# Performance work log

Hardware: AMD Instinct MI355X
Metric: run time of the kernel (lower is better)

## Reference

```python
import jax, jax.numpy as jnp
import numpy as np

# Dimensions per init_kwargs / input_specs
B, N, C = 8192, 4, 2048          # tokens, expansion_rate, hidden_dim
SINKHORN_ITERS = 20
EPS = 1e-5
ALPHA_INIT = 0.01


def setup_inputs() -> dict:
    key = jax.random.key(0)
    k1, k2 = jax.random.split(key)
    return {
        "x_expanded": jax.random.normal(k1, (B, N, C), dtype=jnp.float32),
        "rmsnorm_weight": jnp.ones((C,), dtype=jnp.float32),   # init: ones
        "H_pre": jnp.zeros((N,), dtype=jnp.float32),            # init: zeros
        "H_post": jnp.zeros((N,), dtype=jnp.float32),           # init: zeros
        "H_res": ALPHA_INIT * jax.random.normal(k2, (N, N), dtype=jnp.float32),
    }


def _sinkhorn(M, iters, eps):
    """Iterative row/column normalization -> (approximately) doubly-stochastic."""
    def body(_, M):
        M = M / (jnp.sum(M, axis=1, keepdims=True) + eps)  # row normalize
        M = M / (jnp.sum(M, axis=0, keepdims=True) + eps)  # col normalize
        return M
    return jax.lax.fori_loop(0, iters, body, M)


def reference(x_expanded, rmsnorm_weight, H_pre, H_post, H_res):
    # RMSNorm over hidden dim C, per (token, branch)
    ms = jnp.mean(x_expanded * x_expanded, axis=-1, keepdims=True)  # [B, N, 1]
    x_norm = x_expanded * jax.lax.rsqrt(ms + EPS) * rmsnorm_weight  # [B, N, C]

    # Manifold-constrained residual mixing matrix (doubly stochastic via Sinkhorn)
    H = _sinkhorn(jnp.exp(H_res), SINKHORN_ITERS, EPS)              # [N, N]

    pre = jax.nn.sigmoid(H_pre)    # [N] input-aggregation weights
    post = jax.nn.sigmoid(H_post)  # [N] output-distribution weights

    # Aggregate normalized branches into a single stream, redistribute,
    # and add the Sinkhorn-mixed residual of the raw branches.
    x_agg = jnp.einsum('n,bnc->bc', pre, x_norm)                     # [B, C]
    y = jnp.einsum('mn,bnc->bmc', H, x_expanded) \
        + post[None, :, None] * x_agg[:, None, :]                    # [B, N, C]
    return y
```

## Files before the change

### kernel.cpp

```cpp
#include <hip/hip_runtime.h>
#include <math.h>

#define B_TOK 8192
#define NB 4
#define CH 2048
#define TPB 512
#define SINK_ITERS 20
#define EPS 1e-5f

__global__ void mhc_sinkhorn(const float* __restrict__ H_pre,
                             const float* __restrict__ H_post,
                             const float* __restrict__ H_res,
                             float* __restrict__ ws)
{
    if (threadIdx.x == 0) {
        float M[NB][NB];
        #pragma unroll
        for (int i = 0; i < NB; ++i)
            #pragma unroll
            for (int j = 0; j < NB; ++j)
                M[i][j] = expf(H_res[i * NB + j]);

        for (int it = 0; it < SINK_ITERS; ++it) {
            #pragma unroll
            for (int i = 0; i < NB; ++i) {
                float r = 1.0f / (M[i][0] + M[i][1] + M[i][2] + M[i][3] + EPS);
                #pragma unroll
                for (int j = 0; j < NB; ++j) M[i][j] *= r;
            }
            #pragma unroll
            for (int j = 0; j < NB; ++j) {
                float r = 1.0f / (M[0][j] + M[1][j] + M[2][j] + M[3][j] + EPS);
                #pragma unroll
                for (int i = 0; i < NB; ++i) M[i][j] *= r;
            }
        }
        #pragma unroll
        for (int i = 0; i < NB; ++i)
            #pragma unroll
            for (int j = 0; j < NB; ++j)
                ws[i * NB + j] = M[i][j];
        #pragma unroll
        for (int n = 0; n < NB; ++n) {
            ws[16 + n] = 1.0f / (1.0f + expf(-H_pre[n]));
            ws[20 + n] = 1.0f / (1.0f + expf(-H_post[n]));
        }
    }
}

__global__ __launch_bounds__(TPB) void mhc_main(const float* __restrict__ x,
                                                const float* __restrict__ w,
                                                const float* __restrict__ ws,
                                                float* __restrict__ y)
{
    const int b = blockIdx.x;
    const int t = threadIdx.x;
    const int wave = t >> 6;
    const int lane = t & 63;

    float H[NB][NB], pre[NB], post[NB];
    #pragma unroll
    for (int i = 0; i < NB; ++i)
        #pragma unroll
        for (int j = 0; j < NB; ++j)
            H[i][j] = ws[i * NB + j];
    #pragma unroll
    for (int n = 0; n < NB; ++n) {
        pre[n]  = ws[16 + n];
        post[n] = ws[20 + n];
    }

    const float4* xb = (const float4*)(x + (size_t)b * NB * CH);
    float4 x0 = xb[0 * (CH / 4) + t];
    float4 x1 = xb[1 * (CH / 4) + t];
    float4 x2 = xb[2 * (CH / 4) + t];
    float4 x3 = xb[3 * (CH / 4) + t];

    float4 wv = ((const float4*)w)[t];

    float ss[NB];
    ss[0] = x0.x * x0.x + x0.y * x0.y + x0.z * x0.z + x0.w * x0.w;
    ss[1] = x1.x * x1.x + x1.y * x1.y + x1.z * x1.z + x1.w * x1.w;
    ss[2] = x2.x * x2.x + x2.y * x2.y + x2.z * x2.z + x2.w * x2.w;
    ss[3] = x3.x * x3.x + x3.y * x3.y + x3.z * x3.z + x3.w * x3.w;

    #pragma unroll
    for (int m = 1; m < 64; m <<= 1) {
        #pragma unroll
        for (int n = 0; n < NB; ++n)
            ss[n] += __shfl_xor(ss[n], m);
    }
    __shared__ float red[TPB / 64][NB];
    if (lane == 0) {
        #pragma unroll
        for (int n = 0; n < NB; ++n) red[wave][n] = ss[n];
    }
    __syncthreads();

    float s[NB];
    #pragma unroll
    for (int n = 0; n < NB; ++n) {
        float tot = red[0][n] + red[1][n] + red[2][n] + red[3][n] +
                    red[4][n] + red[5][n] + red[6][n] + red[7][n];
        s[n] = pre[n] * rsqrtf(tot * (1.0f / CH) + EPS);
    }

    float4 wu;
    wu.x = wv.x * (s[0] * x0.x + s[1] * x1.x + s[2] * x2.x + s[3] * x3.x);
    wu.y = wv.y * (s[0] * x0.y + s[1] * x1.y + s[2] * x2.y + s[3] * x3.y);
    wu.z = wv.z * (s[0] * x0.z + s[1] * x1.z + s[2] * x2.z + s[3] * x3.z);
    wu.w = wv.w * (s[0] * x0.w + s[1] * x1.w + s[2] * x2.w + s[3] * x3.w);

    float4* yb = (float4*)(y + (size_t)b * NB * CH);
    #pragma unroll
    for (int m = 0; m < NB; ++m) {
        float4 o;
        o.x = H[m][0] * x0.x + H[m][1] * x1.x + H[m][2] * x2.x + H[m][3] * x3.x + post[m] * wu.x;
        o.y = H[m][0] * x0.y + H[m][1] * x1.y + H[m][2] * x2.y + H[m][3] * x3.y + post[m] * wu.y;
        o.z = H[m][0] * x0.z + H[m][1] * x1.z + H[m][2] * x2.z + H[m][3] * x3.z + post[m] * wu.z;
        o.w = H[m][0] * x0.w + H[m][1] * x1.w + H[m][2] * x2.w + H[m][3] * x3.w + post[m] * wu.w;
        yb[m * (CH / 4) + t] = o;
    }
}

extern "C" void kernel_launch(void* const* d_in, const int* in_sizes, int n_in,
                              void* d_out, int out_size, void* d_ws, size_t ws_size,
                              hipStream_t stream) {
    const float* x      = (const float*)d_in[0];
    const float* wgt    = (const float*)d_in[1];
    const float* h_pre  = (const float*)d_in[2];
    const float* h_post = (const float*)d_in[3];
    const float* h_res  = (const float*)d_in[4];
    float* y  = (float*)d_out;
    float* ws = (float*)d_ws;

    mhc_sinkhorn<<<1, 64, 0, stream>>>(h_pre, h_post, h_res, ws);
    mhc_main<<<B_TOK, TPB, 0, stream>>>(x, wgt, ws, y);
}
```

Measured before the change: 110.0 us.

## Process eight tokens per block with double-buffered loads and nontemporal memory ops

Each block now handles eight tokens instead of one, loading the next token's four branch rows into registers while the current token is reduced and written (two-stage software pipeline). Double-buffered shared reduction slots let one barrier per token suffice. Loads and stores use nontemporal builtins to avoid polluting caches on this streaming workload. This cuts block launch overhead and improves latency hiding, but reduces grid size to 1024 blocks and increases register pressure.

```diff
diff --git a/kernel.cpp b/kernel.cpp
--- a/kernel.cpp
+++ b/kernel.cpp
@@ -5,8 +5,12 @@
 #define NB 4
 #define CH 2048
 #define TPB 512
+#define NBLK 1024
+#define TOK_PER_BLK 8
 #define SINK_ITERS 20
 #define EPS 1e-5f
+
+typedef float f32x4 __attribute__((ext_vector_type(4)));
 
 __global__ void mhc_sinkhorn(const float* __restrict__ H_pre,
                              const float* __restrict__ H_post,
@@ -53,74 +57,112 @@
                                                 const float* __restrict__ ws,
                                                 float* __restrict__ y)
 {
-    const int b = blockIdx.x;
     const int t = threadIdx.x;
     const int wave = t >> 6;
     const int lane = t & 63;
 
-    float H[NB][NB], pre[NB], post[NB];
-    #pragma unroll
-    for (int i = 0; i < NB; ++i)
+    const float H00 = ws[0],  H01 = ws[1],  H02 = ws[2],  H03 = ws[3];
+    const float H10 = ws[4],  H11 = ws[5],  H12 = ws[6],  H13 = ws[7];
+    const float H20 = ws[8],  H21 = ws[9],  H22 = ws[10], H23 = ws[11];
+    const float H30 = ws[12], H31 = ws[13], H32 = ws[14], H33 = ws[15];
+    const float pre0 = ws[16], pre1 = ws[17], pre2 = ws[18], pre3 = ws[19];
+    const float ps0  = ws[20], ps1  = ws[21], ps2  = ws[22], ps3  = ws[23];
+
+    __shared__ f32x4 red4[2][TPB / 64];
+
+    const f32x4 wv = ((const f32x4*)w)[t];
+    const int b0 = blockIdx.x * TOK_PER_BLK;
+
+    auto xload = [&](int b, f32x4& d0, f32x4& d1, f32x4& d2, f32x4& d3) {
+        const f32x4* p = (const f32x4*)x + (size_t)b * (NB * CH / 4) + t;
+        d0 = __builtin_nontemporal_load(p);
+        d1 = __builtin_nontemporal_load(p + (CH / 4));
+        d2 = __builtin_nontemporal_load(p + 2 * (CH / 4));
+        d3 = __builtin_nontemporal_load(p + 3 * (CH / 4));
+    };
+
+    auto process = [&](int b, f32x4 x0, f32x4 x1, f32x4 x2, f32x4 x3, int ph) {
+        float s0 = x0.x * x0.x + x0.y * x0.y + x0.z * x0.z + x0.w * x0.w;
+        float s1 = x1.x * x1.x + x1.y * x1.y + x1.z * x1.z + x1.w * x1.w;
+        float s2 = x2.x * x2.x + x2.y * x2.y + x2.z * x2.z + x2.w * x2.w;
+        float s3 = x3.x * x3.x + x3.y * x3.y + x3.z * x3.z + x3.w * x3.w;
         #pragma unroll
-        for (int j = 0; j < NB; ++j)
-            H[i][j] = ws[i * NB + j];
-    #pragma unroll
-    for (int n = 0; n < NB; ++n) {
-        pre[n]  = ws[16 + n];
-        post[n] = ws[20 + n];
-    }
+        for (int m = 1; m < 64; m <<= 1) {
+            s0 += __shfl_xor(s0, m);
+            s1 += __shfl_xor(s1, m);
+            s2 += __shfl_xor(s2, m);
+            s3 += __shfl_xor(s3, m);
+        }
+        if (lane == 0) {
+            f32x4 v = { s0, s1, s2, s3 };
+            red4[ph][wave] = v;
+        }
 
-    const float4* xb = (const float4*)(x + (size_t)b * NB * CH);
-    float4 x0 = xb[0 * (CH / 4) + t];
-    float4 x1 = xb[1 * (CH / 4) + t];
-    float4 x2 = xb[2 * (CH / 4) + t];
-    float4 x3 = xb[3 * (CH / 4) + t];
+        __builtin_amdgcn_sched_barrier(0);
+        asm volatile("s_waitcnt lgkmcnt(0)" ::: "memory");
+        __builtin_amdgcn_s_barrier();
+        __builtin_amdgcn_sched_barrier(0);
 
-    float4 wv = ((const float4*)w)[t];
+        f32x4 r0 = red4[ph][0], r1 = red4[ph][1], r2 = red4[ph][2], r3 = red4[ph][3];
+        f32x4 r4 = red4[ph][4], r5 = red4[ph][5], r6 = red4[ph][6], r7 = red4[ph][7];
+        float t0 = ((r0.x + r1.x) + (r2.x + r3.x)) + ((r4.x + r5.x) + (r6.x + r7.x));
+        float t1 = ((r0.y + r1.y) + (r2.y + r3.y)) + ((r4.y + r5.y) + (r6.y + r7.y));
+        float t2 = ((r0.z + r1.z) + (r2.z + r3.z)) + ((r4.z + r5.z) + (r6.z + r7.z));
+        float t3 = ((r0.w + r1.w) + (r2.w + r3.w)) + ((r4.w + r5.w) + (r6.w + r7.w));
 
-    float ss[NB];
-    ss[0] = x0.x * x0.x + x0.y * x0.y + x0.z * x0.z + x0.w * x0.w;
-    ss[1] = x1.x * x1.x + x1.y * x1.y + x1.z * x1.z + x1.w * x1.w;
-    ss[2] = x2.x * x2.x + x2.y * x2.y + x2.z * x2.z + x2.w * x2.w;
-    ss[3] = x3.x * x3.x + x3.y * x3.y + x3.z * x3.z + x3.w * x3.w;
+        const float a0 = pre0 * rsqrtf(t0 * (1.0f / CH) + EPS);
+        const float a1 = pre1 * rsqrtf(t1 * (1.0f / CH) + EPS);
+        const float a2 = pre2 * rsqrtf(t2 * (1.0f / CH) + EPS);
+        const float a3 = pre3 * rsqrtf(t3 * (1.0f / CH) + EPS);
 
-    #pragma unroll
-    for (int m = 1; m < 64; m <<= 1) {
-        #pragma unroll
-        for (int n = 0; n < NB; ++n)
-            ss[n] += __shfl_xor(ss[n], m);
-    }
-    __shared__ float red[TPB / 64][NB];
-    if (lane == 0) {
-        #pragma unroll
-        for (int n = 0; n < NB; ++n) red[wave][n] = ss[n];
-    }
-    __syncthreads();
+        f32x4 wu;
+        wu.x = wv.x * (a0 * x0.x + a1 * x1.x + a2 * x2.x + a3 * x3.x);
+        wu.y = wv.y * (a0 * x0.y + a1 * x1.y + a2 * x2.y + a3 * x3.y);
+        wu.z = wv.z * (a0 * x0.z + a1 * x1.z + a2 * x2.z + a3 * x3.z);
+        wu.w = wv.w * (a0 * x0.w + a1 * x1.w + a2 * x2.w + a3 * x3.w);
 
-    float s[NB];
-    #pragma unroll
-    for (int n = 0; n < NB; ++n) {
-        float tot = red[0][n] + red[1][n] + red[2][n] + red[3][n] +
-                    red[4][n] + red[5][n] + red[6][n] + red[7][n];
-        s[n] = pre[n] * rsqrtf(tot * (1.0f / CH) + EPS);
-    }
+        f32x4* yp = (f32x4*)y + (size_t)b * (NB * CH / 4) + t;
+        f32x4 o;
+        o.x = H00 * x0.x + H01 * x1.x + H02 * x2.x + H03 * x3.x + ps0 * wu.x;
+        o.y = H00 * x0.y + H01 * x1.y + H02 * x2.y + H03 * x3.y + ps0 * wu.y;
+        o.z = H00 * x0.z + H01 * x1.z + H02 * x2.z + H03 * x3.z + ps0 * wu.z;
+        o.w = H00 * x0.w + H01 * x1.w + H02 * x2.w + H03 * x3.w + ps0 * wu.w;
+        __builtin_nontemporal_store(o, yp);
+        o.x = H10 * x0.x + H11 * x1.x + H12 * x2.x + H13 * x3.x + ps1 * wu.x;
+        o.y = H10 * x0.y + H11 * x1.y + H12 * x2.y + H13 * x3.y + ps1 * wu.y;
+        o.z = H10 * x0.z + H11 * x1.z + H12 * x2.z + H13 * x3.z + ps1 * wu.z;
+        o.w = H10 * x0.w + H11 * x1.w + H12 * x2.w + H13 * x3.w + ps1 * wu.w;
+        __builtin_nontemporal_store(o, yp + (CH / 4));
+        o.x = H20 * x0.x + H21 * x1.x + H22 * x2.x + H23 * x3.x + ps2 * wu.x;
+        o.y = H20 * x0.y + H21 * x1.y + H22 * x2.y + H23 * x3.y + ps2 * wu.y;
+        o.z = H20 * x0.z + H21 * x1.z + H22 * x2.z + H23 * x3.z + ps2 * wu.z;
+        o.w = H20 * x0.w + H21 * x1.w + H22 * x2.w + H23 * x3.w + ps2 * wu.w;
+        __builtin_nontemporal_store(o, yp + 2 * (CH / 4));
+        o.x = H30 * x0.x + H31 * x1.x + H32 * x2.x + H33 * x3.x + ps3 * wu.x;
+        o.y = H30 * x0.y + H31 * x1.y + H32 * x2.y + H33 * x3.y + ps3 * wu.y;
+        o.z = H30 * x0.z + H31 * x1.z + H32 * x2.z + H33 * x3.z + ps3 * wu.z;
+        o.w = H30 * x0.w + H31 * x1.w + H32 * x2.w + H33 * x3.w + ps3 * wu.w;
+        __builtin_nontemporal_store(o, yp + 3 * (CH / 4));
+    };
 
-    float4 wu;
-    wu.x = wv.x * (s[0] * x0.x + s[1] * x1.x + s[2] * x2.x + s[3] * x3.x);
-    wu.y = wv.y * (s[0] * x0.y + s[1] * x1.y + s[2] * x2.y + s[3] * x3.y);
-    wu.z = wv.z * (s[0] * x0.z + s[1] * x1.z + s[2] * x2.z + s[3] * x3.z);
-    wu.w = wv.w * (s[0] * x0.w + s[1] * x1.w + s[2] * x2.w + s[3] * x3.w);
+    f32x4 xA0, xA1, xA2, xA3, xB0, xB1, xB2, xB3;
 
-    float4* yb = (float4*)(y + (size_t)b * NB * CH);
-    #pragma unroll
-    for (int m = 0; m < NB; ++m) {
-        float4 o;
-        o.x = H[m][0] * x0.x + H[m][1] * x1.x + H[m][2] * x2.x + H[m][3] * x3.x + post[m] * wu.x;
-        o.y = H[m][0] * x0.y + H[m][1] * x1.y + H[m][2] * x2.y + H[m][3] * x3.y + post[m] * wu.y;
-        o.z = H[m][0] * x0.z + H[m][1] * x1.z + H[m][2] * x2.z + H[m][3] * x3.z + post[m] * wu.z;
-        o.w = H[m][0] * x0.w + H[m][1] * x1.w + H[m][2] * x2.w + H[m][3] * x3.w + post[m] * wu.w;
-        yb[m * (CH / 4) + t] = o;
-    }
+    xload(b0 + 0, xA0, xA1, xA2, xA3);
+    xload(b0 + 1, xB0, xB1, xB2, xB3);
+    process(b0 + 0, xA0, xA1, xA2, xA3, 0);
+    xload(b0 + 2, xA0, xA1, xA2, xA3);
+    process(b0 + 1, xB0, xB1, xB2, xB3, 1);
+    xload(b0 + 3, xB0, xB1, xB2, xB3);
+    process(b0 + 2, xA0, xA1, xA2, xA3, 0);
+    xload(b0 + 4, xA0, xA1, xA2, xA3);
+    process(b0 + 3, xB0, xB1, xB2, xB3, 1);
+    xload(b0 + 5, xB0, xB1, xB2, xB3);
+    process(b0 + 4, xA0, xA1, xA2, xA3, 0);
+    xload(b0 + 6, xA0, xA1, xA2, xA3);
+    process(b0 + 5, xB0, xB1, xB2, xB3, 1);
+    xload(b0 + 7, xB0, xB1, xB2, xB3);
+    process(b0 + 6, xA0, xA1, xA2, xA3, 0);
+    process(b0 + 7, xB0, xB1, xB2, xB3, 1);
 }
 
 extern "C" void kernel_launch(void* const* d_in, const int* in_sizes, int n_in,
@@ -135,5 +177,5 @@
     float* ws = (float*)d_ws;
 
     mhc_sinkhorn<<<1, 64, 0, stream>>>(h_pre, h_post, h_res, ws);
-    mhc_main<<<B_TOK, TPB, 0, stream>>>(x, wgt, ws, y);
+    mhc_main<<<NBLK, TPB, 0, stream>>>(x, wgt, ws, y);
 }
```

Measured after the change: 108.2 us. No clear change (-1.7%).
